# Kernel optimization log

Hardware: AMD Instinct MI355X
Metric: run time of the kernel (lower is better)

## Reference

```python
import jax, jax.numpy as jnp
import numpy as np

B, S, D = 2, 2048, 1024
H = 16
HD = D // H  # 64


def setup_inputs() -> dict:
    key = jax.random.key(0)
    ks = jax.random.split(key, 6)
    sc = 1.0 / np.sqrt(D)
    x = jax.random.normal(ks[0], (B, S, D), dtype=jnp.float32)
    Wq = jax.random.normal(ks[1], (D, D), dtype=jnp.float32) * sc
    Wk = jax.random.normal(ks[2], (D, D), dtype=jnp.float32) * sc
    Wv = jax.random.normal(ks[3], (D, D), dtype=jnp.float32) * sc
    Wo = jax.random.normal(ks[4], (D, D), dtype=jnp.float32) * sc
    bo = jax.random.normal(ks[5], (D,), dtype=jnp.float32) * 0.01
    return {"x": x, "Wq": Wq, "Wk": Wk, "Wv": Wv, "Wo": Wo, "bo": bo}


def reference(x, Wq, Wk, Wv, Wo, bo):
    # projections: [B,S,D] -> [B,H,S,HD]
    def split_heads(t):
        return t.reshape(B, S, H, HD).transpose(0, 2, 1, 3)

    q = split_heads(x @ Wq)
    k = split_heads(x @ Wk)
    v = split_heads(x @ Wv)

    # naive full score matrix [B,H,S,S], masked causal, scaled softmax
    scores = jnp.einsum("bhqd,bhkd->bhqk", q, k)
    causal = jnp.tril(jnp.ones((S, S), dtype=bool))  # True = keep
    scores = jnp.where(causal, scores, -jnp.inf)
    attn = jax.nn.softmax(scores / np.sqrt(HD), axis=-1)

    ctx = jnp.einsum("bhqk,bhkd->bhqd", attn, v)  # [B,H,S,HD]
    ctx = ctx.transpose(0, 2, 1, 3).reshape(B, S, D)
    return ctx @ Wo + bo
```

## Files before the change

### kernel.cpp

```cpp
#include <hip/hip_runtime.h>

#define BB 2
#define SS 2048
#define DD 1024
#define HH 16
#define HD 64
#define MM (BB*SS)

typedef __bf16 bf16x8 __attribute__((ext_vector_type(8)));
typedef short  s16x4  __attribute__((ext_vector_type(4)));
typedef float  f32x4  __attribute__((ext_vector_type(4)));

#ifndef __has_builtin
#define __has_builtin(x) 0
#endif

__device__ __forceinline__ unsigned short f2bf(float f) {
    unsigned int u = __float_as_uint(f);
    u = (u + 0x7fffu + ((u >> 16) & 1u)) >> 16;
    return (unsigned short)u;
}
__device__ __forceinline__ unsigned int pack2(float a, float b) {
    return (unsigned int)f2bf(a) | ((unsigned int)f2bf(b) << 16);
}
__device__ __forceinline__ unsigned int pack2_fast(float a, float b) {
#if __has_builtin(__builtin_amdgcn_perm)
    return __builtin_amdgcn_perm(__float_as_uint(b) + 0x8000u,
                                 __float_as_uint(a) + 0x8000u, 0x07060302u);
#else
    return ((__float_as_uint(a) + 0x8000u) >> 16) |
           ((__float_as_uint(b) + 0x8000u) & 0xffff0000u);
#endif
}

__device__ __forceinline__ void gload_lds16(const unsigned short* g, unsigned short* l) {
    __builtin_amdgcn_global_load_lds(
        (const __attribute__((address_space(1))) void*)g,
        (__attribute__((address_space(3))) void*)l, 16, 0, 0);
}

__global__ __launch_bounds__(256) void prep_kernel(const float* __restrict__ x,
                                                   const float* __restrict__ Wq,
                                                   const float* __restrict__ Wk,
                                                   const float* __restrict__ Wv,
                                                   const float* __restrict__ Wo,
                                                   unsigned short* __restrict__ Xb,
                                                   unsigned short* __restrict__ Wqkvt,
                                                   unsigned short* __restrict__ Wot) {
    __shared__ float tile[32][33];
    const int bx = blockIdx.x;
    const int t = threadIdx.x;
    if (bx < 2048) {
        int gid = bx * 256 + t;
        int i = gid * 8;
        float4 a = *(const float4*)(x + i);
        float4 b = *(const float4*)(x + i + 4);
        uint4 o;
        o.x = pack2(a.x, a.y); o.y = pack2(a.z, a.w);
        o.z = pack2(b.x, b.y); o.w = pack2(b.z, b.w);
        ((uint4*)Xb)[gid] = o;
        return;
    }
    int pb = bx - 2048;
    int p = pb >> 10, rem = pb & 1023;
    int bxx = rem & 31, byy = rem >> 5;
    const float* src = (p == 0) ? Wq : (p == 1) ? Wk : (p == 2) ? Wv : Wo;
    unsigned short* dst = (p == 3) ? Wot : (Wqkvt + (size_t)p * DD * DD);
    int tx = t & 31, ty = t >> 5;
    int n = bxx * 32 + tx;
#pragma unroll
    for (int i = 0; i < 4; ++i) {
        int k = byy * 32 + ty + i * 8;
        tile[ty + i * 8][tx] = src[k * DD + n];
    }
    __syncthreads();
#pragma unroll
    for (int i = 0; i < 4; ++i) {
        int n2 = bxx * 32 + ty + i * 8;
        int k2 = byy * 32 + tx;
        dst[n2 * DD + k2] = f2bf(tile[tx][ty + i * 8]);
    }
}

#define GEMM_K_LOOP(Aglob, Bglob)                                                 \
    __shared__ unsigned short smem[128 * 132];                                    \
    unsigned short (*As)[64]  = (unsigned short(*)[64])smem;                      \
    unsigned short (*Bs)[64]  = (unsigned short(*)[64])(smem + 128 * 64);         \
    unsigned short (*Es)[132] = (unsigned short(*)[132])smem;                     \
    const int n0 = blockIdx.x * 128, m0 = blockIdx.y * 128;                       \
    const int t = threadIdx.x;                                                    \
    const int wave = t >> 6, lane = t & 63;                                       \
    const int wm = wave >> 1, wn = wave & 1;                                      \
    const int l15 = lane & 15, quad = lane >> 4;                                  \
    const int lr = lane >> 3, lg = (lane & 7);                                    \
    const int lc = (lg ^ lr) * 8;                    \
    f32x4 acc[4][4];                                                              \
    _Pragma("unroll") for (int i = 0; i < 4; ++i)                                 \
        _Pragma("unroll") for (int j = 0; j < 4; ++j) acc[i][j] = f32x4{0,0,0,0}; \
    for (int kt = 0; kt < 16; ++kt) {                                             \
        if (kt) __syncthreads();                                                  \
        _Pragma("unroll") for (int i = 0; i < 4; ++i) {                           \
            int row = wave * 32 + i * 8;                                          \
            gload_lds16(Aglob + (size_t)(m0 + row + lr) * DD + kt * 64 + lc, &As[row][0]); \
            gload_lds16(Bglob + (size_t)(n0 + row + lr) * DD + kt * 64 + lc, &Bs[row][0]); \
        }                                                                         \
        __syncthreads();                                                          \
        _Pragma("unroll") for (int kh = 0; kh < 2; ++kh) {                        \
            bf16x8 af[4], bfr[4];                                                 \
            _Pragma("unroll") for (int s = 0; s < 4; ++s)                         \
                af[s] = *(const bf16x8*)&As[wm * 64 + s * 16 + l15][((kh * 4 + quad) ^ (l15 & 7)) * 8]; \
            _Pragma("unroll") for (int s = 0; s < 4; ++s)                         \
                bfr[s] = *(const bf16x8*)&Bs[wn * 64 + s * 16 + l15][((kh * 4 + quad) ^ (l15 & 7)) * 8]; \
            _Pragma("unroll") for (int i = 0; i < 4; ++i)                         \
                _Pragma("unroll") for (int j = 0; j < 4; ++j)                     \
                    acc[i][j] = __builtin_amdgcn_mfma_f32_16x16x32_bf16(af[i], bfr[j], acc[i][j], 0, 0, 0); \
        }                                                                         \
    }                                                                             \
    __syncthreads();

__global__ __launch_bounds__(256) void qkv_gemm_kernel(const unsigned short* __restrict__ Xb,
                                                       const unsigned short* __restrict__ Wt,
                                                       unsigned short* __restrict__ Qg,
                                                       unsigned short* __restrict__ Kg,
                                                       unsigned short* __restrict__ Vt) {
    GEMM_K_LOOP(Xb, Wt)
    const int p = n0 >> 10;
    const float qs = (p == 0) ? 0.18033688011112042f : 1.0f;
    if (p < 2) {
#pragma unroll
        for (int sm = 0; sm < 4; ++sm)
#pragma unroll
            for (int sn = 0; sn < 4; ++sn)
#pragma unroll
                for (int i = 0; i < 4; ++i)
                    Es[wm * 64 + sm * 16 + quad * 4 + i][wn * 64 + sn * 16 + l15] = f2bf(acc[sm][sn][i] * qs);
    } else {
#pragma unroll
        for (int sm = 0; sm < 4; ++sm)
#pragma unroll
            for (int sn = 0; sn < 4; ++sn)
#pragma unroll
                for (int i = 0; i < 4; ++i)
                    Es[wn * 64 + sn * 16 + l15][wm * 64 + sm * 16 + quad * 4 + i] = f2bf(acc[sm][sn][i]);
    }
    __syncthreads();
    const int h0 = (n0 & 1023) >> 6;
    if (p < 2) {
        unsigned short* dst0 = p ? Kg : Qg;
        int ml = t >> 1, seg = t & 1;
        int gm = m0 + ml, b = gm >> 11, s = gm & 2047;
        unsigned short* dptr = dst0 + ((size_t)(b * HH + h0 + seg) * SS + s) * HD;
#pragma unroll
        for (int j = 0; j < 8; ++j)
            *(uint4*)(dptr + j * 8) = *(const uint4*)&Es[ml][seg * 64 + j * 8];
    } else {
        int nl = t >> 1, mh = t & 1;
        int h = h0 + (nl >> 6), hd = nl & 63;
        int b = m0 >> 11, s0 = (m0 & 2047) + mh * 64;
        unsigned short* dptr = Vt + ((size_t)(b * HH + h) * HD + hd) * SS + s0;
#pragma unroll
        for (int j = 0; j < 8; ++j)
            *(uint4*)(dptr + j * 8) = *(const uint4*)&Es[nl][mh * 64 + j * 8];
    }
}

__global__ __launch_bounds__(256) void out_gemm_kernel(const unsigned short* __restrict__ Ctxb,
                                                       const unsigned short* __restrict__ Wot,
                                                       const float* __restrict__ bo,
                                                       float* __restrict__ out) {
    GEMM_K_LOOP(Ctxb, Wot)
    (void)Es;
#pragma unroll
    for (int sn = 0; sn < 4; ++sn) {
        int gn = n0 + wn * 64 + sn * 16 + l15;
        float bias = bo[gn];
#pragma unroll
        for (int sm = 0; sm < 4; ++sm)
#pragma unroll
            for (int i = 0; i < 4; ++i) {
                int gm = m0 + wm * 64 + sm * 16 + quad * 4 + i;
                out[(size_t)gm * DD + gn] = acc[sm][sn][i] + bias;
            }
    }
}

__global__ __launch_bounds__(256) void attn_kernel(const unsigned short* __restrict__ Qg,
                                                   const unsigned short* __restrict__ Kg,
                                                   const unsigned short* __restrict__ Vt,
                                                   unsigned short* __restrict__ Ctxb) {
    __shared__ unsigned short Ks[2][128][64];
    __shared__ unsigned short Vs[2][64][128];

    const int bh = blockIdx.x;
    const int qt = (int)gridDim.y - 1 - (int)blockIdx.y;
    const int t = threadIdx.x;
    const int wave = t >> 6, lane = t & 63;
    const int l15 = lane & 15, quad = lane >> 4;
    const int q0 = qt * 128;
    const int b = bh >> 4, h = bh & 15;

    const unsigned short* Qb = Qg + (size_t)bh * SS * HD;
    const unsigned short* Kb = Kg + (size_t)bh * SS * HD;
    const unsigned short* Vb = Vt + (size_t)bh * HD * SS;

    int qrow[2];
    bf16x8 bq[2][2];
#pragma unroll
    for (int qf = 0; qf < 2; ++qf) {
        qrow[qf] = q0 + wave * 32 + qf * 16 + l15;
#pragma unroll
        for (int hh = 0; hh < 2; ++hh)
            bq[qf][hh] = *(const bf16x8*)(Qb + (size_t)qrow[qf] * HD + hh * 32 + quad * 8);
    }

    const int rloc = lane >> 3, pcl = lane & 7;
    const int vrl = lane >> 4, vgc = lane & 15;
    const unsigned short* ksrc[4];
    const unsigned short* vsrc[4];
#pragma unroll
    for (int j = 0; j < 4; ++j) {
        int krow = (wave * 4 + j) * 8 + rloc;
        ksrc[j] = Kb + (size_t)krow * HD + (pcl ^ rloc) * 8;
        int vrow = wave * 16 + j * 4 + vrl;
        vsrc[j] = Vb + (size_t)vrow * SS + (vgc ^ (vrow & 15)) * 8;
    }

    f32x4 acc[2][4];
#pragma unroll
    for (int qf = 0; qf < 2; ++qf)
#pragma unroll
        for (int db = 0; db < 4; ++db) acc[qf][db] = f32x4{0,0,0,0};
    f32x4 accl[2] = {f32x4{0,0,0,0}, f32x4{0,0,0,0}};
    const s16x4 ones = {(short)0x3F80, (short)0x3F80, (short)0x3F80, (short)0x3F80};
    const int nkt = qt + 1;

#pragma unroll
    for (int j = 0; j < 4; ++j) {
        gload_lds16(ksrc[j], &Ks[0][(wave * 4 + j) * 8][0]);
        gload_lds16(vsrc[j], &Vs[0][wave * 16 + j * 4][0]);
    }
    __syncthreads();

    for (int kt = 0; kt < nkt; ++kt) {
        const int buf = kt & 1;
        const int k0 = kt * 128;
        if (kt + 1 < nkt) {
            const int nb = buf ^ 1;
#pragma unroll
            for (int j = 0; j < 4; ++j) {
                gload_lds16(ksrc[j] + (size_t)(kt + 1) * 128 * HD, &Ks[nb][(wave * 4 + j) * 8][0]);
                gload_lds16(vsrc[j] + (kt + 1) * 128,              &Vs[nb][wave * 16 + j * 4][0]);
            }
        }

        const bool tail = (kt == nkt - 1);
#pragma unroll
        for (int kb = 0; kb < 8; ++kb) {
            f32x4 St[2] = {f32x4{0,0,0,0}, f32x4{0,0,0,0}};
#pragma unroll
            for (int hh = 0; hh < 2; ++hh) {
                bf16x8 ak = *(const bf16x8*)&Ks[buf][kb * 16 + l15][((hh * 4 + quad) ^ (l15 & 7)) * 8];
                St[0] = __builtin_amdgcn_mfma_f32_16x16x32_bf16(ak, bq[0][hh], St[0], 0, 0, 0);
                St[1] = __builtin_amdgcn_mfma_f32_16x16x32_bf16(ak, bq[1][hh], St[1], 0, 0, 0);
            }
            if (tail) {
#pragma unroll
                for (int qf = 0; qf < 2; ++qf)
#pragma unroll
                    for (int r = 0; r < 4; ++r)
                        if (k0 + kb * 16 + quad * 4 + r > qrow[qf]) St[qf][r] = -1e30f;
            }
            s16x4 ap[2];
#pragma unroll
            for (int qf = 0; qf < 2; ++qf) {
                float e0 = __builtin_amdgcn_exp2f(St[qf][0]);
                float e1 = __builtin_amdgcn_exp2f(St[qf][1]);
                float e2 = __builtin_amdgcn_exp2f(St[qf][2]);
                float e3 = __builtin_amdgcn_exp2f(St[qf][3]);
                uint2 uu;
                uu.x = pack2_fast(e0, e1);
                uu.y = pack2_fast(e2, e3);
                ap[qf] = *(s16x4*)&uu;
            }
#pragma unroll
            for (int db = 0; db < 4; ++db) {
                const int pg = (2 * kb + (quad >> 1)) ^ l15;
                s16x4 bv = *(const s16x4*)&Vs[buf][db * 16 + l15][pg * 8 + (quad & 1) * 4];
                acc[0][db] = __builtin_amdgcn_mfma_f32_16x16x16bf16_1k(ap[0], bv, acc[0][db], 0, 0, 0);
                acc[1][db] = __builtin_amdgcn_mfma_f32_16x16x16bf16_1k(ap[1], bv, acc[1][db], 0, 0, 0);
            }
            accl[0] = __builtin_amdgcn_mfma_f32_16x16x16bf16_1k(ap[0], ones, accl[0], 0, 0, 0);
            accl[1] = __builtin_amdgcn_mfma_f32_16x16x16bf16_1k(ap[1], ones, accl[1], 0, 0, 0);
        }

        __syncthreads();
    }

#pragma unroll
    for (int qf = 0; qf < 2; ++qf) {
#pragma unroll
        for (int r = 0; r < 4; ++r) {
            float ir = 1.0f / accl[qf][r];
            int gq = q0 + wave * 32 + qf * 16 + quad * 4 + r;
            size_t base = ((size_t)(b * SS + gq)) * DD + h * HD;
#pragma unroll
            for (int db = 0; db < 4; ++db)
                Ctxb[base + db * 16 + l15] = f2bf(acc[qf][db][r] * ir);
        }
    }
}

extern "C" void kernel_launch(void* const* d_in, const int* in_sizes, int n_in,
                              void* d_out, int out_size, void* d_ws, size_t ws_size,
                              hipStream_t stream) {
    const float* x  = (const float*)d_in[0];
    const float* Wq = (const float*)d_in[1];
    const float* Wk = (const float*)d_in[2];
    const float* Wv = (const float*)d_in[3];
    const float* Wo = (const float*)d_in[4];
    const float* bo = (const float*)d_in[5];
    float* out = (float*)d_out;

    char* w = (char*)d_ws;
    unsigned short* Xb    = (unsigned short*)(w);
    unsigned short* Wqkvt = (unsigned short*)(w + (size_t)(8 << 20));
    unsigned short* Wot   = (unsigned short*)(w + (size_t)(14 << 20));
    unsigned short* Qg    = (unsigned short*)(w + (size_t)(16 << 20));
    unsigned short* Kg    = (unsigned short*)(w + (size_t)(24 << 20));
    unsigned short* Vt    = (unsigned short*)(w + (size_t)(32 << 20));
    unsigned short* Ctxb  = (unsigned short*)(w + (size_t)(40 << 20));

    prep_kernel<<<6144, 256, 0, stream>>>(x, Wq, Wk, Wv, Wo, Xb, Wqkvt, Wot);
    qkv_gemm_kernel<<<dim3(3 * DD / 128, MM / 128), 256, 0, stream>>>(Xb, Wqkvt, Qg, Kg, Vt);
    attn_kernel<<<dim3(BB * HH, SS / 128), 256, 0, stream>>>(Qg, Kg, Vt, Ctxb);
    out_gemm_kernel<<<dim3(DD / 128, MM / 128), 256, 0, stream>>>(Ctxb, Wot, bo, out);
}
```

Before: 178.6 us.

## Pair low and high 64-row query tiles per block for causal load balance

Each attention block now handles two 64-row query tiles, one from the start and one from the end of the sequence, so every block does nearly the same amount of causal work. The KV loop runs to the longer tile's extent and skips 16-key sub-blocks that are fully masked for both tiles, with per-tile MFMA predication. This targets the tail imbalance of the old one-tile-per-block causal schedule and adds branch and predication overhead in the inner loop.

```diff
diff --git a/kernel.cpp b/kernel.cpp
--- a/kernel.cpp
+++ b/kernel.cpp
@@ -192,25 +192,29 @@
     __shared__ unsigned short Vs[2][64][128];
 
     const int bh = blockIdx.x;
-    const int qt = (int)gridDim.y - 1 - (int)blockIdx.y;
+    const int pi = blockIdx.y;
     const int t = threadIdx.x;
     const int wave = t >> 6, lane = t & 63;
     const int l15 = lane & 15, quad = lane >> 4;
-    const int q0 = qt * 128;
+    const int q0A = pi * 64;
+    const int q0B = (31 - pi) * 64;
+    const int aIters = (pi + 2) >> 1;
+    const int bIters = (33 - pi) >> 1;
     const int b = bh >> 4, h = bh & 15;
 
     const unsigned short* Qb = Qg + (size_t)bh * SS * HD;
     const unsigned short* Kb = Kg + (size_t)bh * SS * HD;
     const unsigned short* Vb = Vt + (size_t)bh * HD * SS;
 
-    int qrow[2];
+    const int qrow0 = q0A + wave * 16 + l15;
+    const int qrow1 = q0B + wave * 16 + l15;
+    const int qA_hi = q0A + wave * 16 + 15;
+    const int qB_hi = q0B + wave * 16 + 15;
     bf16x8 bq[2][2];
 #pragma unroll
-    for (int qf = 0; qf < 2; ++qf) {
-        qrow[qf] = q0 + wave * 32 + qf * 16 + l15;
-#pragma unroll
-        for (int hh = 0; hh < 2; ++hh)
-            bq[qf][hh] = *(const bf16x8*)(Qb + (size_t)qrow[qf] * HD + hh * 32 + quad * 8);
+    for (int hh = 0; hh < 2; ++hh) {
+        bq[0][hh] = *(const bf16x8*)(Qb + (size_t)qrow0 * HD + hh * 32 + quad * 8);
+        bq[1][hh] = *(const bf16x8*)(Qb + (size_t)qrow1 * HD + hh * 32 + quad * 8);
     }
 
     const int rloc = lane >> 3, pcl = lane & 7;
@@ -232,7 +236,6 @@
         for (int db = 0; db < 4; ++db) acc[qf][db] = f32x4{0,0,0,0};
     f32x4 accl[2] = {f32x4{0,0,0,0}, f32x4{0,0,0,0}};
     const s16x4 ones = {(short)0x3F80, (short)0x3F80, (short)0x3F80, (short)0x3F80};
-    const int nkt = qt + 1;
 
 #pragma unroll
     for (int j = 0; j < 4; ++j) {
@@ -241,10 +244,10 @@
     }
     __syncthreads();
 
-    for (int kt = 0; kt < nkt; ++kt) {
+    for (int kt = 0; kt < bIters; ++kt) {
         const int buf = kt & 1;
         const int k0 = kt * 128;
-        if (kt + 1 < nkt) {
+        if (kt + 1 < bIters) {
             const int nb = buf ^ 1;
 #pragma unroll
             for (int j = 0; j < 4; ++j) {
@@ -253,23 +256,42 @@
             }
         }
 
-        const bool tail = (kt == nkt - 1);
+        const bool diagA = (kt == aIters - 1);
+        const bool diagB = (kt == bIters - 1);
+        const bool inA = (kt < aIters);
 #pragma unroll
         for (int kb = 0; kb < 8; ++kb) {
+            const int kbase = k0 + kb * 16;
+            const bool a0 = inA && (kbase <= qA_hi);
+            const bool a1 = (kbase <= qB_hi);
+            if (!a0 && !a1) continue;
+            bf16x8 ak[2];
+#pragma unroll
+            for (int hh = 0; hh < 2; ++hh)
+                ak[hh] = *(const bf16x8*)&Ks[buf][kb * 16 + l15][((hh * 4 + quad) ^ (l15 & 7)) * 8];
+
             f32x4 St[2] = {f32x4{0,0,0,0}, f32x4{0,0,0,0}};
-#pragma unroll
-            for (int hh = 0; hh < 2; ++hh) {
-                bf16x8 ak = *(const bf16x8*)&Ks[buf][kb * 16 + l15][((hh * 4 + quad) ^ (l15 & 7)) * 8];
-                St[0] = __builtin_amdgcn_mfma_f32_16x16x32_bf16(ak, bq[0][hh], St[0], 0, 0, 0);
-                St[1] = __builtin_amdgcn_mfma_f32_16x16x32_bf16(ak, bq[1][hh], St[1], 0, 0, 0);
-            }
-            if (tail) {
-#pragma unroll
-                for (int qf = 0; qf < 2; ++qf)
+            if (a0) {
+#pragma unroll
+                for (int hh = 0; hh < 2; ++hh)
+                    St[0] = __builtin_amdgcn_mfma_f32_16x16x32_bf16(ak[hh], bq[0][hh], St[0], 0, 0, 0);
+                if (diagA) {
 #pragma unroll
                     for (int r = 0; r < 4; ++r)
-                        if (k0 + kb * 16 + quad * 4 + r > qrow[qf]) St[qf][r] = -1e30f;
-            }
+                        if (kbase + quad * 4 + r > qrow0) St[0][r] = -1e30f;
+                }
+            }
+            if (a1) {
+#pragma unroll
+                for (int hh = 0; hh < 2; ++hh)
+                    St[1] = __builtin_amdgcn_mfma_f32_16x16x32_bf16(ak[hh], bq[1][hh], St[1], 0, 0, 0);
+                if (diagB) {
+#pragma unroll
+                    for (int r = 0; r < 4; ++r)
+                        if (kbase + quad * 4 + r > qrow1) St[1][r] = -1e30f;
+                }
+            }
+
             s16x4 ap[2];
 #pragma unroll
             for (int qf = 0; qf < 2; ++qf) {
@@ -282,15 +304,16 @@
                 uu.y = pack2_fast(e2, e3);
                 ap[qf] = *(s16x4*)&uu;
             }
+
 #pragma unroll
             for (int db = 0; db < 4; ++db) {
                 const int pg = (2 * kb + (quad >> 1)) ^ l15;
                 s16x4 bv = *(const s16x4*)&Vs[buf][db * 16 + l15][pg * 8 + (quad & 1) * 4];
-                acc[0][db] = __builtin_amdgcn_mfma_f32_16x16x16bf16_1k(ap[0], bv, acc[0][db], 0, 0, 0);
-                acc[1][db] = __builtin_amdgcn_mfma_f32_16x16x16bf16_1k(ap[1], bv, acc[1][db], 0, 0, 0);
-            }
-            accl[0] = __builtin_amdgcn_mfma_f32_16x16x16bf16_1k(ap[0], ones, accl[0], 0, 0, 0);
-            accl[1] = __builtin_amdgcn_mfma_f32_16x16x16bf16_1k(ap[1], ones, accl[1], 0, 0, 0);
+                if (a0) acc[0][db] = __builtin_amdgcn_mfma_f32_16x16x16bf16_1k(ap[0], bv, acc[0][db], 0, 0, 0);
+                if (a1) acc[1][db] = __builtin_amdgcn_mfma_f32_16x16x16bf16_1k(ap[1], bv, acc[1][db], 0, 0, 0);
+            }
+            if (a0) accl[0] = __builtin_amdgcn_mfma_f32_16x16x16bf16_1k(ap[0], ones, accl[0], 0, 0, 0);
+            if (a1) accl[1] = __builtin_amdgcn_mfma_f32_16x16x16bf16_1k(ap[1], ones, accl[1], 0, 0, 0);
         }
 
         __syncthreads();
@@ -298,10 +321,11 @@
 
 #pragma unroll
     for (int qf = 0; qf < 2; ++qf) {
+        const int qb0 = (qf == 0) ? q0A : q0B;
 #pragma unroll
         for (int r = 0; r < 4; ++r) {
             float ir = 1.0f / accl[qf][r];
-            int gq = q0 + wave * 32 + qf * 16 + quad * 4 + r;
+            int gq = qb0 + wave * 16 + quad * 4 + r;
             size_t base = ((size_t)(b * SS + gq)) * DD + h * HD;
 #pragma unroll
             for (int db = 0; db < 4; ++db)
@@ -332,6 +356,6 @@
 
     prep_kernel<<<6144, 256, 0, stream>>>(x, Wq, Wk, Wv, Wo, Xb, Wqkvt, Wot);
     qkv_gemm_kernel<<<dim3(3 * DD / 128, MM / 128), 256, 0, stream>>>(Xb, Wqkvt, Qg, Kg, Vt);
-    attn_kernel<<<dim3(BB * HH, SS / 128), 256, 0, stream>>>(Qg, Kg, Vt, Ctxb);
+    attn_kernel<<<dim3(BB * HH, 16), 256, 0, stream>>>(Qg, Kg, Vt, Ctxb);
     out_gemm_kernel<<<dim3(DD / 128, MM / 128), 256, 0, stream>>>(Ctxb, Wot, bo, out);
 }
```

Result: slower. 207.2 us (+16.0%).
